# Kernel tuning notes

Hardware: AMD Instinct MI355X
Metric: run time of the kernel (lower is better)

The kernel has to match this reference:

```python
import jax, jax.numpy as jnp
import numpy as np
import math

B, S, D, H = 2, 2048, 1024, 16

def setup_inputs() -> dict:
    key = jax.random.key(0)
    ks = jax.random.split(key, 13)
    def lin(kw, kb, out_d, in_d):
        W = jax.random.normal(kw, (out_d, in_d), dtype=jnp.float32) * 0.02
        b = jax.random.normal(kb, (out_d,), dtype=jnp.float32) * 0.02
        return W, b
    Wq, bq = lin(ks[0], ks[1], D, D)
    Wk, bk = lin(ks[2], ks[3], D, D)
    Wv, bv = lin(ks[4], ks[5], D, D)
    Wo, bo = lin(ks[6], ks[7], D, D)
    query = jax.random.normal(ks[8], (B, S, D), dtype=jnp.float32)
    key_t = jax.random.normal(ks[9], (B, S, D), dtype=jnp.float32)
    value = jax.random.normal(ks[10], (B, S, D), dtype=jnp.float32)
    src_mask = jax.random.randint(ks[11], (B, S), 0, 2).astype(bool)  # True = masked out
    return {"query": query, "key": key_t, "value": value, "src_mask": src_mask,
            "Wq": Wq, "bq": bq, "Wk": Wk, "bk": bk, "Wv": Wv, "bv": bv,
            "Wo": Wo, "bo": bo, "nhead": H}

def reference(query, key, value, src_mask, Wq, bq, Wk, bk, Wv, bv, Wo, bo, nhead):
    b, s, d = query.shape
    hd = d // nhead
    scale = 1.0 / math.sqrt(hd)
    def split_heads(x):  # [b,s,d] -> [b,h,s,hd]
        return x.reshape(b, -1, nhead, hd).transpose(0, 2, 1, 3)
    q = split_heads(query @ Wq.T + bq)
    k = split_heads(key @ Wk.T + bk)
    v = split_heads(value @ Wv.T + bv)
    scores = jnp.einsum('bhqe,bhke->bhqk', q, k) * scale  # [b,h,s,s]
    # mask True -> -9e9, broadcast over heads and query positions (matches repeat)
    scores = jnp.where(src_mask[:, None, None, :], jnp.float32(-9e9), scores)
    probs = jax.nn.softmax(scores, axis=-1)
    # dropout is identity in eval mode
    out = jnp.einsum('bhqk,bhke->bhqe', probs, v)  # [b,h,s,hd]
    out = out.transpose(0, 2, 1, 3).reshape(b, s, d)
    out = out @ Wo.T + bo
    return out
```

## Files before the change

### kernel.cpp

```cpp
#include <hip/hip_runtime.h>
#include <hip/hip_bf16.h>
#include <cstdint>
#include <cstddef>

#define B_ 2
#define S_ 2048
#define D_ 1024
#define H_ 16
#define HD_ 64
#define M_ 4096

typedef __attribute__((ext_vector_type(8))) short short8;
typedef __attribute__((ext_vector_type(4))) short shortx4;
typedef __attribute__((ext_vector_type(4))) float floatx4;

__device__ __forceinline__ floatx4 mfma32(short8 a, short8 b, floatx4 c) {
    return __builtin_amdgcn_mfma_f32_16x16x32_bf16(a, b, c, 0, 0, 0);
}
__device__ __forceinline__ floatx4 mfma16(shortx4 a, shortx4 b, floatx4 c) {
    return __builtin_amdgcn_mfma_f32_16x16x16bf16_1k(a, b, c, 0, 0, 0);
}

__device__ __forceinline__ void gload_lds16(const __hip_bfloat16* g, __hip_bfloat16* lds_base) {
    __builtin_amdgcn_global_load_lds(
        (const __attribute__((address_space(1))) void*)g,
        (__attribute__((address_space(3))) void*)lds_base, 16, 0, 0);
}

__global__ __launch_bounds__(256) void cvt3_kernel(
    const float* __restrict__ a, const float* __restrict__ b, const float* __restrict__ c,
    __hip_bfloat16* __restrict__ dst, int n)
{
    const float* src = blockIdx.z == 0 ? a : blockIdx.z == 1 ? b : c;
    __hip_bfloat16* d = dst + (size_t)blockIdx.z * n;
    int i = (blockIdx.x * 256 + threadIdx.x) * 4;
    float4 v = *(const float4*)(src + i);
    union { __hip_bfloat16 h[4]; uint2 u; } cv;
    cv.h[0] = __float2bfloat16(v.x); cv.h[1] = __float2bfloat16(v.y);
    cv.h[2] = __float2bfloat16(v.z); cv.h[3] = __float2bfloat16(v.w);
    *(uint2*)(d + i) = cv.u;
}

__global__ __launch_bounds__(256) void cvt4_kernel(
    const float* __restrict__ a, const float* __restrict__ b,
    const float* __restrict__ c, const float* __restrict__ e,
    __hip_bfloat16* __restrict__ dst, int n)
{
    const float* src = blockIdx.z == 0 ? a : blockIdx.z == 1 ? b : blockIdx.z == 2 ? c : e;
    __hip_bfloat16* d = dst + (size_t)blockIdx.z * n;
    int i = (blockIdx.x * 256 + threadIdx.x) * 4;
    float4 v = *(const float4*)(src + i);
    union { __hip_bfloat16 h[4]; uint2 u; } cv;
    cv.h[0] = __float2bfloat16(v.x); cv.h[1] = __float2bfloat16(v.y);
    cv.h[2] = __float2bfloat16(v.z); cv.h[3] = __float2bfloat16(v.w);
    *(uint2*)(d + i) = cv.u;
}

template <int MODE>
__device__ __forceinline__ void gemm_core(
    const __hip_bfloat16* __restrict__ A,
    const __hip_bfloat16* __restrict__ W,
    const float* __restrict__ bias,
    void* __restrict__ Cout,
    __hip_bfloat16* __restrict__ smem,
    int m0, int n0, int N)
{
    __hip_bfloat16* As = smem;
    __hip_bfloat16* Bs = smem + 128 * 32;
    const int K = D_;
    const int tid  = threadIdx.x;
    const int wave = tid >> 6;
    const int lane = tid & 63;
    const int quad = lane >> 4;
    const int l15  = lane & 15;
    const int wm   = (wave & 1) * 64;
    const int wn   = (wave >> 1) * 64;
    const int srow = lane >> 2;
    const int scol = (lane & 3) * 8;

    floatx4 acc[4][4];
#pragma unroll
    for (int i = 0; i < 4; i++)
#pragma unroll
        for (int j = 0; j < 4; j++) {
            floatx4 z = {0.f, 0.f, 0.f, 0.f};
            acc[i][j] = z;
        }

    for (int k0 = 0; k0 < K; k0 += 32) {
        __syncthreads();
#pragma unroll
        for (int t = 0; t < 2; t++) {
            int r0 = wave * 32 + t * 16;
            gload_lds16(A + (size_t)(m0 + r0 + srow) * K + k0 + scol, As + r0 * 32);
            gload_lds16(W + (size_t)(n0 + r0 + srow) * K + k0 + scol, Bs + r0 * 32);
        }
        __syncthreads();

        short8 afr[4], bfr[4];
#pragma unroll
        for (int i = 0; i < 4; i++)
            afr[i] = *(const short8*)(As + (wm + i * 16 + l15) * 32 + quad * 8);
#pragma unroll
        for (int j = 0; j < 4; j++)
            bfr[j] = *(const short8*)(Bs + (wn + j * 16 + l15) * 32 + quad * 8);
#pragma unroll
        for (int i = 0; i < 4; i++)
#pragma unroll
            for (int j = 0; j < 4; j++)
                acc[i][j] = mfma32(afr[i], bfr[j], acc[i][j]);
    }

    if constexpr (MODE == 1) {
#pragma unroll
        for (int j = 0; j < 4; j++) {
            int col = n0 + wn + j * 16 + l15;
            int h = col >> 6, e = col & 63;
            float bv = bias[col];
#pragma unroll
            for (int i = 0; i < 4; i++) {
                int s0 = m0 + wm + i * 16 + quad * 4;
                int bb = s0 >> 11, sl = s0 & 2047;
                union { __hip_bfloat16 hx[4]; uint2 u; } pk;
#pragma unroll
                for (int r = 0; r < 4; r++)
                    pk.hx[r] = __float2bfloat16(acc[i][j][r] + bv);
                *(uint2*)((__hip_bfloat16*)Cout + (((size_t)bb * H_ + h) * HD_ + e) * S_ + sl) = pk.u;
            }
        }
    } else {
#pragma unroll
        for (int j = 0; j < 4; j++) {
            int col = n0 + wn + j * 16 + l15;
            float bv = bias[col];
#pragma unroll
            for (int i = 0; i < 4; i++) {
#pragma unroll
                for (int r = 0; r < 4; r++) {
                    int rowg = m0 + wm + i * 16 + quad * 4 + r;
                    float val = acc[i][j][r] + bv;
                    if constexpr (MODE == 0)
                        ((__hip_bfloat16*)Cout)[(size_t)rowg * N + col] = __float2bfloat16(val);
                    else
                        ((float*)Cout)[(size_t)rowg * N + col] = val;
                }
            }
        }
    }
}

__global__ __launch_bounds__(256) void qkv_gemm_kernel(
    const __hip_bfloat16* __restrict__ qb, const __hip_bfloat16* __restrict__ kb,
    const __hip_bfloat16* __restrict__ vb,
    const __hip_bfloat16* __restrict__ Wqb, const __hip_bfloat16* __restrict__ Wkb,
    const __hip_bfloat16* __restrict__ Wvb,
    const float* __restrict__ bq, const float* __restrict__ bk, const float* __restrict__ bv,
    __hip_bfloat16* __restrict__ Qp, __hip_bfloat16* __restrict__ Kp,
    __hip_bfloat16* __restrict__ Vt)
{
    __shared__ __hip_bfloat16 smem[2 * 128 * 32] __attribute__((aligned(16)));
    const int z = blockIdx.z;
    const __hip_bfloat16* A = z == 0 ? qb : z == 1 ? kb : vb;
    const __hip_bfloat16* W = z == 0 ? Wqb : z == 1 ? Wkb : Wvb;
    const float* bias = z == 0 ? bq : z == 1 ? bk : bv;
    int m0 = blockIdx.y * 128, n0 = blockIdx.x * 128;
    if (z < 2) gemm_core<0>(A, W, bias, z == 0 ? (void*)Qp : (void*)Kp, smem, m0, n0, D_);
    else       gemm_core<1>(A, W, bias, (void*)Vt, smem, m0, n0, D_);
}

__global__ __launch_bounds__(256) void oproj_gemm_kernel(
    const __hip_bfloat16* __restrict__ A, const __hip_bfloat16* __restrict__ Wob,
    const float* __restrict__ bo, float* __restrict__ out)
{
    __shared__ __hip_bfloat16 smem[2 * 128 * 32] __attribute__((aligned(16)));
    gemm_core<2>(A, Wob, bo, (void*)out, smem, blockIdx.y * 128, blockIdx.x * 128, D_);
}

#define LDP 72
__global__ __launch_bounds__(256) void flash_attn_kernel(
    const __hip_bfloat16* __restrict__ Q,
    const __hip_bfloat16* __restrict__ Kp,
    const __hip_bfloat16* __restrict__ Vt,
    const int* __restrict__ mask,
    __hip_bfloat16* __restrict__ O)
{
    __shared__ __hip_bfloat16 Qs [128 * LDP] __attribute__((aligned(16)));
    __shared__ __hip_bfloat16 Ks [64 * LDP]  __attribute__((aligned(16)));
    __shared__ __hip_bfloat16 Vts[64 * LDP]  __attribute__((aligned(16)));

    const int tid  = threadIdx.x;
    const int q0   = blockIdx.x * 128;
    const int bh   = blockIdx.y;
    const int b    = bh >> 4;
    const int h    = bh & 15;
    const int wave = tid >> 6;
    const int lane = tid & 63;
    const int quad = lane >> 4;
    const int l15  = lane & 15;
    const float kSc = 0.18033688f;

    const size_t baseQ = ((size_t)b * S_ + q0) * D_ + (size_t)h * HD_;
#pragma unroll
    for (int c = tid; c < 1024; c += 256) {
        int row = c >> 3, kc = c & 7;
        *(uint4*)(Qs + row * LDP + kc * 8) = *(const uint4*)(Q + baseQ + (size_t)row * D_ + kc * 8);
    }
    __syncthreads();

    short8 qb[2][2];
#pragma unroll
    for (int qt = 0; qt < 2; qt++)
#pragma unroll
        for (int h2 = 0; h2 < 2; h2++)
            qb[qt][h2] = *(const short8*)(Qs + (wave * 32 + qt * 16 + l15) * LDP + h2 * 32 + quad * 8);

    float lsum[2] = {0.f, 0.f};
    floatx4 o_acc[2][4];
#pragma unroll
    for (int qt = 0; qt < 2; qt++)
#pragma unroll
        for (int ot = 0; ot < 4; ot++) {
            floatx4 z = {0.f, 0.f, 0.f, 0.f};
            o_acc[qt][ot] = z;
        }

    const int* mrow = mask + b * S_;
    const __hip_bfloat16* VtBase = Vt + (size_t)bh * HD_ * S_;

    for (int kv0 = 0; kv0 < S_; kv0 += 64) {
        __syncthreads();
        const size_t baseK = ((size_t)b * S_ + kv0) * D_ + (size_t)h * HD_;
#pragma unroll
        for (int c = tid; c < 512; c += 256) {
            int row = c >> 3, kc = c & 7;
            *(uint4*)(Ks + row * LDP + kc * 8) =
                *(const uint4*)(Kp + baseK + (size_t)row * D_ + kc * 8);
            *(uint4*)(Vts + row * LDP + kc * 8) =
                *(const uint4*)(VtBase + (size_t)row * S_ + kv0 + kc * 8);
        }
        __syncthreads();

        int4 mq[4];
#pragma unroll
        for (int nt = 0; nt < 4; nt++)
            mq[nt] = *(const int4*)(mrow + kv0 + nt * 16 + quad * 4);

        floatx4 s_acc[2][4];
#pragma unroll
        for (int nt = 0; nt < 4; nt++) {
            short8 kb0 = *(const short8*)(Ks + (nt * 16 + l15) * LDP + quad * 8);
            short8 kb1 = *(const short8*)(Ks + (nt * 16 + l15) * LDP + 32 + quad * 8);
#pragma unroll
            for (int qt = 0; qt < 2; qt++) {
                floatx4 z = {0.f, 0.f, 0.f, 0.f};
                z = mfma32(kb0, qb[qt][0], z);
                z = mfma32(kb1, qb[qt][1], z);
                s_acc[qt][nt] = z;
            }
        }

        shortx4 pf[2][4];
#pragma unroll
        for (int qt = 0; qt < 2; qt++) {
#pragma unroll
            for (int nt = 0; nt < 4; nt++) {
                float pe0 = mq[nt].x ? 0.f : __builtin_amdgcn_exp2f(s_acc[qt][nt][0] * kSc);
                float pe1 = mq[nt].y ? 0.f : __builtin_amdgcn_exp2f(s_acc[qt][nt][1] * kSc);
                float pe2 = mq[nt].z ? 0.f : __builtin_amdgcn_exp2f(s_acc[qt][nt][2] * kSc);
                float pe3 = mq[nt].w ? 0.f : __builtin_amdgcn_exp2f(s_acc[qt][nt][3] * kSc);
                lsum[qt] += (pe0 + pe1) + (pe2 + pe3);
                union { shortx4 s4; __hip_bfloat162 b2[2]; } pk;
                pk.b2[0] = __float22bfloat162_rn({pe0, pe1});
                pk.b2[1] = __float22bfloat162_rn({pe2, pe3});
                pf[qt][nt] = pk.s4;
            }
        }

#pragma unroll
        for (int nt = 0; nt < 4; nt++) {
#pragma unroll
            for (int ot = 0; ot < 4; ot++) {
                shortx4 vb = *(const shortx4*)(Vts + (ot * 16 + l15) * LDP + nt * 16 + quad * 4);
#pragma unroll
                for (int qt = 0; qt < 2; qt++)
                    o_acc[qt][ot] = mfma16(pf[qt][nt], vb, o_acc[qt][ot]);
            }
        }
    }

#pragma unroll
    for (int qt = 0; qt < 2; qt++) {
        lsum[qt] += __shfl_xor(lsum[qt], 16);
        lsum[qt] += __shfl_xor(lsum[qt], 32);
    }

    const size_t baseO = ((size_t)b * S_ + q0) * D_ + (size_t)h * HD_;
#pragma unroll
    for (int qt = 0; qt < 2; qt++) {
#pragma unroll
        for (int r = 0; r < 4; r++) {
            float inv = 1.0f / __shfl(lsum[qt], quad * 4 + r);
            int rowl = wave * 32 + qt * 16 + quad * 4 + r;
#pragma unroll
            for (int ot = 0; ot < 4; ot++)
                O[baseO + (size_t)rowl * D_ + ot * 16 + l15] =
                    __float2bfloat16(o_acc[qt][ot][r] * inv);
        }
    }
}

extern "C" void kernel_launch(void* const* d_in, const int* in_sizes, int n_in,
                              void* d_out, int out_size, void* d_ws, size_t ws_size,
                              hipStream_t stream) {
    const float* query = (const float*)d_in[0];
    const float* key   = (const float*)d_in[1];
    const float* value = (const float*)d_in[2];
    const int*   mask  = (const int*)d_in[3];
    const float* Wq    = (const float*)d_in[4];
    const float* bq    = (const float*)d_in[5];
    const float* Wk    = (const float*)d_in[6];
    const float* bk    = (const float*)d_in[7];
    const float* Wv    = (const float*)d_in[8];
    const float* bv    = (const float*)d_in[9];
    const float* Wo    = (const float*)d_in[10];
    const float* bo    = (const float*)d_in[11];
    float* out = (float*)d_out;

    const size_t SZ_IN = (size_t)M_ * D_;
    const size_t SZ_W  = (size_t)D_ * D_;
    __hip_bfloat16* qb  = (__hip_bfloat16*)d_ws;
    __hip_bfloat16* kb  = qb  + SZ_IN;
    __hip_bfloat16* vb  = kb  + SZ_IN;
    __hip_bfloat16* Wqb = vb  + SZ_IN;
    __hip_bfloat16* Wkb = Wqb + SZ_W;
    __hip_bfloat16* Wvb = Wkb + SZ_W;
    __hip_bfloat16* Wob = Wvb + SZ_W;
    __hip_bfloat16* Qp  = Wob + SZ_W;
    __hip_bfloat16* Kp  = Qp  + SZ_IN;
    __hip_bfloat16* Vt  = Kp  + SZ_IN;

    cvt3_kernel<<<dim3(SZ_IN / 1024, 1, 3), 256, 0, stream>>>(query, key, value, qb, (int)SZ_IN);
    cvt4_kernel<<<dim3(SZ_W / 1024, 1, 4), 256, 0, stream>>>(Wq, Wk, Wv, Wo, Wqb, (int)SZ_W);

    qkv_gemm_kernel<<<dim3(D_ / 128, M_ / 128, 3), 256, 0, stream>>>(
        qb, kb, vb, Wqb, Wkb, Wvb, bq, bk, bv, Qp, Kp, Vt);

    flash_attn_kernel<<<dim3(S_ / 128, B_ * H_), 256, 0, stream>>>(Qp, Kp, Vt, mask, Qp);

    oproj_gemm_kernel<<<dim3(D_ / 128, M_ / 128), 256, 0, stream>>>(Qp, Wob, bo, out);
}
```

Baseline: 251.5 us.

## Use 8 waves per flash-attention block and 64-row tiles for output projection

The flash-attention kernel now runs 512 threads per block, with each wave owning 16 query rows instead of 32. This halves per-wave registers and spreads each K/V tile load over more threads. The output projection gets its own kernel with 64x128 tiles, doubling the grid from 256 blocks to 512 to fill more compute units, at the cost of more weight re-reads. The generic GEMM core drops its fp32 store path since only bf16 outputs remain.

Measured after the change: 239.5 us. -4.8%, faster.

```diff
diff --git a/kernel.cpp b/kernel.cpp
--- a/kernel.cpp
+++ b/kernel.cpp
@@ -138,11 +138,8 @@
 #pragma unroll
                 for (int r = 0; r < 4; r++) {
                     int rowg = m0 + wm + i * 16 + quad * 4 + r;
-                    float val = acc[i][j][r] + bv;
-                    if constexpr (MODE == 0)
-                        ((__hip_bfloat16*)Cout)[(size_t)rowg * N + col] = __float2bfloat16(val);
-                    else
-                        ((float*)Cout)[(size_t)rowg * N + col] = val;
+                    ((__hip_bfloat16*)Cout)[(size_t)rowg * N + col] =
+                        __float2bfloat16(acc[i][j][r] + bv);
                 }
             }
         }
@@ -169,15 +166,77 @@
 }
 
 __global__ __launch_bounds__(256) void oproj_gemm_kernel(
-    const __hip_bfloat16* __restrict__ A, const __hip_bfloat16* __restrict__ Wob,
-    const float* __restrict__ bo, float* __restrict__ out)
-{
-    __shared__ __hip_bfloat16 smem[2 * 128 * 32] __attribute__((aligned(16)));
-    gemm_core<2>(A, Wob, bo, (void*)out, smem, blockIdx.y * 128, blockIdx.x * 128, D_);
+    const __hip_bfloat16* __restrict__ A, const __hip_bfloat16* __restrict__ W,
+    const float* __restrict__ bias, float* __restrict__ out)
+{
+    __shared__ __hip_bfloat16 As[64 * 32]  __attribute__((aligned(16)));
+    __shared__ __hip_bfloat16 Bs[128 * 32] __attribute__((aligned(16)));
+    const int K = D_, N = D_;
+    const int tid  = threadIdx.x;
+    const int m0   = blockIdx.y * 64;
+    const int n0   = blockIdx.x * 128;
+    const int wave = tid >> 6;
+    const int lane = tid & 63;
+    const int quad = lane >> 4;
+    const int l15  = lane & 15;
+    const int wm   = (wave & 1) * 32;
+    const int wn   = (wave >> 1) * 64;
+    const int srow = lane >> 2;
+    const int scol = (lane & 3) * 8;
+
+    floatx4 acc[2][4];
+#pragma unroll
+    for (int i = 0; i < 2; i++)
+#pragma unroll
+        for (int j = 0; j < 4; j++) {
+            floatx4 z = {0.f, 0.f, 0.f, 0.f};
+            acc[i][j] = z;
+        }
+
+    for (int k0 = 0; k0 < K; k0 += 32) {
+        __syncthreads();
+        {
+            int ra = wave * 16;
+            gload_lds16(A + (size_t)(m0 + ra + srow) * K + k0 + scol, As + ra * 32);
+#pragma unroll
+            for (int t = 0; t < 2; t++) {
+                int rb = wave * 32 + t * 16;
+                gload_lds16(W + (size_t)(n0 + rb + srow) * K + k0 + scol, Bs + rb * 32);
+            }
+        }
+        __syncthreads();
+
+        short8 afr[2], bfr[4];
+#pragma unroll
+        for (int i = 0; i < 2; i++)
+            afr[i] = *(const short8*)(As + (wm + i * 16 + l15) * 32 + quad * 8);
+#pragma unroll
+        for (int j = 0; j < 4; j++)
+            bfr[j] = *(const short8*)(Bs + (wn + j * 16 + l15) * 32 + quad * 8);
+#pragma unroll
+        for (int i = 0; i < 2; i++)
+#pragma unroll
+            for (int j = 0; j < 4; j++)
+                acc[i][j] = mfma32(afr[i], bfr[j], acc[i][j]);
+    }
+
+#pragma unroll
+    for (int j = 0; j < 4; j++) {
+        int col = n0 + wn + j * 16 + l15;
+        float bv = bias[col];
+#pragma unroll
+        for (int i = 0; i < 2; i++) {
+#pragma unroll
+            for (int r = 0; r < 4; r++) {
+                int rowg = m0 + wm + i * 16 + quad * 4 + r;
+                out[(size_t)rowg * N + col] = acc[i][j][r] + bv;
+            }
+        }
+    }
 }
 
 #define LDP 72
-__global__ __launch_bounds__(256) void flash_attn_kernel(
+__global__ __launch_bounds__(512) void flash_attn_kernel(
     const __hip_bfloat16* __restrict__ Q,
     const __hip_bfloat16* __restrict__ Kp,
     const __hip_bfloat16* __restrict__ Vt,
@@ -201,28 +260,23 @@
 
     const size_t baseQ = ((size_t)b * S_ + q0) * D_ + (size_t)h * HD_;
 #pragma unroll
-    for (int c = tid; c < 1024; c += 256) {
+    for (int c = tid; c < 1024; c += 512) {
         int row = c >> 3, kc = c & 7;
         *(uint4*)(Qs + row * LDP + kc * 8) = *(const uint4*)(Q + baseQ + (size_t)row * D_ + kc * 8);
     }
     __syncthreads();
 
-    short8 qb[2][2];
-#pragma unroll
-    for (int qt = 0; qt < 2; qt++)
-#pragma unroll
-        for (int h2 = 0; h2 < 2; h2++)
-            qb[qt][h2] = *(const short8*)(Qs + (wave * 32 + qt * 16 + l15) * LDP + h2 * 32 + quad * 8);
-
-    float lsum[2] = {0.f, 0.f};
-    floatx4 o_acc[2][4];
-#pragma unroll
-    for (int qt = 0; qt < 2; qt++)
-#pragma unroll
-        for (int ot = 0; ot < 4; ot++) {
-            floatx4 z = {0.f, 0.f, 0.f, 0.f};
-            o_acc[qt][ot] = z;
-        }
+    short8 qb[2];
+    qb[0] = *(const short8*)(Qs + (wave * 16 + l15) * LDP + quad * 8);
+    qb[1] = *(const short8*)(Qs + (wave * 16 + l15) * LDP + 32 + quad * 8);
+
+    float lsum = 0.f;
+    floatx4 o_acc[4];
+#pragma unroll
+    for (int ot = 0; ot < 4; ot++) {
+        floatx4 z = {0.f, 0.f, 0.f, 0.f};
+        o_acc[ot] = z;
+    }
 
     const int* mrow = mask + b * S_;
     const __hip_bfloat16* VtBase = Vt + (size_t)bh * HD_ * S_;
@@ -230,9 +284,8 @@
     for (int kv0 = 0; kv0 < S_; kv0 += 64) {
         __syncthreads();
         const size_t baseK = ((size_t)b * S_ + kv0) * D_ + (size_t)h * HD_;
-#pragma unroll
-        for (int c = tid; c < 512; c += 256) {
-            int row = c >> 3, kc = c & 7;
+        {
+            int row = tid >> 3, kc = tid & 7;
             *(uint4*)(Ks + row * LDP + kc * 8) =
                 *(const uint4*)(Kp + baseK + (size_t)row * D_ + kc * 8);
             *(uint4*)(Vts + row * LDP + kc * 8) =
@@ -245,35 +298,29 @@
         for (int nt = 0; nt < 4; nt++)
             mq[nt] = *(const int4*)(mrow + kv0 + nt * 16 + quad * 4);
 
-        floatx4 s_acc[2][4];
+        floatx4 s_acc[4];
 #pragma unroll
         for (int nt = 0; nt < 4; nt++) {
             short8 kb0 = *(const short8*)(Ks + (nt * 16 + l15) * LDP + quad * 8);
             short8 kb1 = *(const short8*)(Ks + (nt * 16 + l15) * LDP + 32 + quad * 8);
-#pragma unroll
-            for (int qt = 0; qt < 2; qt++) {
-                floatx4 z = {0.f, 0.f, 0.f, 0.f};
-                z = mfma32(kb0, qb[qt][0], z);
-                z = mfma32(kb1, qb[qt][1], z);
-                s_acc[qt][nt] = z;
-            }
-        }
-
-        shortx4 pf[2][4];
-#pragma unroll
-        for (int qt = 0; qt < 2; qt++) {
-#pragma unroll
-            for (int nt = 0; nt < 4; nt++) {
-                float pe0 = mq[nt].x ? 0.f : __builtin_amdgcn_exp2f(s_acc[qt][nt][0] * kSc);
-                float pe1 = mq[nt].y ? 0.f : __builtin_amdgcn_exp2f(s_acc[qt][nt][1] * kSc);
-                float pe2 = mq[nt].z ? 0.f : __builtin_amdgcn_exp2f(s_acc[qt][nt][2] * kSc);
-                float pe3 = mq[nt].w ? 0.f : __builtin_amdgcn_exp2f(s_acc[qt][nt][3] * kSc);
-                lsum[qt] += (pe0 + pe1) + (pe2 + pe3);
-                union { shortx4 s4; __hip_bfloat162 b2[2]; } pk;
-                pk.b2[0] = __float22bfloat162_rn({pe0, pe1});
-                pk.b2[1] = __float22bfloat162_rn({pe2, pe3});
-                pf[qt][nt] = pk.s4;
-            }
+            floatx4 z = {0.f, 0.f, 0.f, 0.f};
+            z = mfma32(kb0, qb[0], z);
+            z = mfma32(kb1, qb[1], z);
+            s_acc[nt] = z;
+        }
+
+        shortx4 pf[4];
+#pragma unroll
+        for (int nt = 0; nt < 4; nt++) {
+            float pe0 = mq[nt].x ? 0.f : __builtin_amdgcn_exp2f(s_acc[nt][0] * kSc);
+            float pe1 = mq[nt].y ? 0.f : __builtin_amdgcn_exp2f(s_acc[nt][1] * kSc);
+            float pe2 = mq[nt].z ? 0.f : __builtin_amdgcn_exp2f(s_acc[nt][2] * kSc);
+            float pe3 = mq[nt].w ? 0.f : __builtin_amdgcn_exp2f(s_acc[nt][3] * kSc);
+            lsum += (pe0 + pe1) + (pe2 + pe3);
+            union { shortx4 s4; __hip_bfloat162 b2[2]; } pk;
+            pk.b2[0] = __float22bfloat162_rn({pe0, pe1});
+            pk.b2[1] = __float22bfloat162_rn({pe2, pe3});
+            pf[nt] = pk.s4;
         }
 
 #pragma unroll
@@ -281,31 +328,23 @@
 #pragma unroll
             for (int ot = 0; ot < 4; ot++) {
                 shortx4 vb = *(const shortx4*)(Vts + (ot * 16 + l15) * LDP + nt * 16 + quad * 4);
-#pragma unroll
-                for (int qt = 0; qt < 2; qt++)
-                    o_acc[qt][ot] = mfma16(pf[qt][nt], vb, o_acc[qt][ot]);
-            }
-        }
-    }
-
-#pragma unroll
-    for (int qt = 0; qt < 2; qt++) {
-        lsum[qt] += __shfl_xor(lsum[qt], 16);
-        lsum[qt] += __shfl_xor(lsum[qt], 32);
-    }
+                o_acc[ot] = mfma16(pf[nt], vb, o_acc[ot]);
+            }
+        }
+    }
+
+    lsum += __shfl_xor(lsum, 16);
+    lsum += __shfl_xor(lsum, 32);
 
     const size_t baseO = ((size_t)b * S_ + q0) * D_ + (size_t)h * HD_;
 #pragma unroll
-    for (int qt = 0; qt < 2; qt++) {
-#pragma unroll
-        for (int r = 0; r < 4; r++) {
-            float inv = 1.0f / __shfl(lsum[qt], quad * 4 + r);
-            int rowl = wave * 32 + qt * 16 + quad * 4 + r;
-#pragma unroll
-            for (int ot = 0; ot < 4; ot++)
-                O[baseO + (size_t)rowl * D_ + ot * 16 + l15] =
-                    __float2bfloat16(o_acc[qt][ot][r] * inv);
-        }
+    for (int r = 0; r < 4; r++) {
+        float inv = 1.0f / __shfl(lsum, quad * 4 + r);
+        int rowl = wave * 16 + quad * 4 + r;
+#pragma unroll
+        for (int ot = 0; ot < 4; ot++)
+            O[baseO + (size_t)rowl * D_ + ot * 16 + l15] =
+                __float2bfloat16(o_acc[ot][r] * inv);
     }
 }
 
@@ -345,7 +384,7 @@
     qkv_gemm_kernel<<<dim3(D_ / 128, M_ / 128, 3), 256, 0, stream>>>(
         qb, kb, vb, Wqb, Wkb, Wvb, bq, bk, bv, Qp, Kp, Vt);
 
-    flash_attn_kernel<<<dim3(S_ / 128, B_ * H_), 256, 0, stream>>>(Qp, Kp, Vt, mask, Qp);
-
-    oproj_gemm_kernel<<<dim3(D_ / 128, M_ / 128), 256, 0, stream>>>(Qp, Wob, bo, out);
-}
+    flash_attn_kernel<<<dim3(S_ / 128, B_ * H_), 512, 0, stream>>>(Qp, Kp, Vt, mask, Qp);
+
+    oproj_gemm_kernel<<<dim3(D_ / 128, M_ / 64), 256, 0, stream>>>(Qp, Wob, bo, out);
+}
```
